# Performance work log

Measured on AMD Instinct MI355X. Metric: run time of the kernel, lower is better.

## Reference

```python
import jax, jax.numpy as jnp
import numpy as np


def setup_inputs() -> dict:
    key = jax.random.key(0)
    k1, k2 = jax.random.split(key)
    embedding = jax.random.normal(k1, (8192, 256), dtype=jnp.float32)
    label = jax.random.randint(k2, (8192,), 0, 1000, dtype=jnp.int64 if jax.config.jax_enable_x64 else jnp.int32)
    return {"embedding": embedding, "label": label}


def reference(embedding, label):
    # embedding: [B, W]; label is unused by the original module's math.
    B, W = embedding.shape
    miu = embedding.mean(axis=0)                      # [W]
    ec = embedding - miu                              # [B, W] centered
    # mean over batch of outer products ec[b] ec[b]^T == (ec^T @ ec) / B
    cov = jnp.einsum('bi,bj->ij', ec, ec) / B         # [W, W]
    diff = cov - jnp.eye(W, dtype=embedding.dtype)
    loss = jnp.sqrt(jnp.sum(diff * diff))             # Frobenius norm
    return loss
```

## Files before the change

### kernel.cpp

```cpp
#include <hip/hip_runtime.h>
#include <math.h>

typedef unsigned int uint32;
typedef unsigned short u16;
typedef __bf16 bf16x8 __attribute__((ext_vector_type(8)));
typedef float f32x16 __attribute__((ext_vector_type(16)));

#define BROWS 8192
#define WDIM 256
#define NT 3
#define CHUNKS 64
#define TILE_ELEMS 16384
#define FIN_BLOCKS 192

#define WS_LOSS 16384
#define WS_DONE 16385
#define WS_PART 16640

__device__ __forceinline__ uint32 pack2bf(float lo, float hi) {
    uint32 a = __float_as_uint(lo), b = __float_as_uint(hi);
    a = (a + 0x7FFFu + ((a >> 16) & 1u)) >> 16;
    b = (b + 0x7FFFu + ((b >> 16) & 1u)) >> 16;
    return (a & 0xFFFFu) | (b << 16);
}
__device__ __forceinline__ u16 f2bf(float x) {
    uint32 a = __float_as_uint(x);
    return (u16)((a + 0x7FFFu + ((a >> 16) & 1u)) >> 16);
}
__device__ __forceinline__ float bflo(uint32 v) { return __uint_as_float(v << 16); }
__device__ __forceinline__ float bfhi(uint32 v) { return __uint_as_float(v & 0xFFFF0000u); }

__device__ __forceinline__ int uswz(int col, int krp) {
    return col * 64 + ((((krp >> 2) ^ (col & 15)) << 2) | (krp & 3));
}

__global__ __launch_bounds__(256)
void gram_fused(const float* __restrict__ E, float* __restrict__ ws) {
    __shared__ uint32 U[WDIM * 64];
    const int t = blockIdx.x, c = blockIdx.y;
    const int tid = threadIdx.x;
    const int ncg = (t == 1) ? 4 : 2;
    const int gcol0 = (t == 2) ? 128 : 0;
    const int row0 = c * 128;
    const int c4 = tid & 15, rp = tid >> 4;

    if (t == 0 && c == 0 && tid < 2) ws[WS_LOSS + tid] = 0.0f;

    for (int cg = 0; cg < ncg; ++cg) {
        const float* Eb = E + (size_t)row0 * WDIM + gcol0 + cg * 64;
        float4 fa[4], fb[4];
        #pragma unroll
        for (int p = 0; p < 4; ++p) {
            const int r0 = 2 * (rp + 16 * p);
            fa[p] = *(const float4*)(Eb + (size_t)r0 * WDIM + c4 * 4);
            fb[p] = *(const float4*)(Eb + (size_t)(r0 + 1) * WDIM + c4 * 4);
        }
        #pragma unroll
        for (int p = 0; p < 4; ++p) {
            const int krp = rp + 16 * p;
            const int colb = cg * 64 + c4 * 4;
            const float av[4] = {fa[p].x, fa[p].y, fa[p].z, fa[p].w};
            const float bv[4] = {fb[p].x, fb[p].y, fb[p].z, fb[p].w};
            #pragma unroll
            for (int i = 0; i < 4; ++i)
                U[uswz(colb + i, krp)] = pack2bf(av[i], bv[i]);
        }
    }
    __syncthreads();

    if (t == 1) {
        const int col = tid;
        float s = 0.f;
        #pragma unroll
        for (int g = 0; g < 16; ++g) {
            const uint4 v = *(const uint4*)&U[col * 64 + ((g ^ (col & 15)) << 2)];
            s += bflo(v.x) + bfhi(v.x) + bflo(v.y) + bfhi(v.y)
               + bflo(v.z) + bfhi(v.z) + bflo(v.w) + bfhi(v.w);
        }
        ws[c * WDIM + col] = s;
    }

    const int w = tid >> 6, l = tid & 63, lm = l & 31;
    const int bBase = (t == 1) ? 128 : 0;
    const int colA = w * 32 + lm;

    f32x16 acc[4];
    #pragma unroll
    for (int n = 0; n < 4; ++n)
        #pragma unroll
        for (int r = 0; r < 16; ++r) acc[n][r] = 0.f;

    #pragma unroll
    for (int s8 = 0; s8 < 8; ++s8) {
        const int grp = 2 * s8 + (l >> 5);
        const bf16x8 a = *(const bf16x8*)&U[colA * 64 + ((grp ^ (colA & 15)) << 2)];
        #pragma unroll
        for (int n = 0; n < 4; ++n) {
            const int colB = bBase + n * 32 + lm;
            const bf16x8 b = *(const bf16x8*)&U[colB * 64 + ((grp ^ (colB & 15)) << 2)];
            acc[n] = __builtin_amdgcn_mfma_f32_32x32x16_bf16(a, b, acc[n], 0, 0, 0);
        }
    }

    u16* part = (u16*)(ws + WS_PART);
    u16* dst = part + ((size_t)c * NT + t) * TILE_ELEMS;
    const int rbase = 32 * w + 4 * (l >> 5);
    #pragma unroll
    for (int n = 0; n < 4; ++n)
        #pragma unroll
        for (int r = 0; r < 16; ++r) {
            const int row = rbase + (r & 3) + 8 * (r >> 2);
            dst[row * 128 + n * 32 + lm] = f2bf(acc[n][r]);
        }
}

__global__ __launch_bounds__(256)
void finalize_kernel(float* __restrict__ ws, float* __restrict__ out) {
    __shared__ float mu[WDIM];
    __shared__ float red[4];
    const u16* part = (const u16*)(ws + WS_PART);
    float* lossacc = ws + WS_LOSS;
    unsigned* done = (unsigned*)(ws + WS_DONE);
    const int tid = threadIdx.x;

    {
        float s = 0.f;
        #pragma unroll 8
        for (int c = 0; c < CHUNKS; ++c) s += ws[c * WDIM + tid];
        mu[tid] = s * (1.0f / (float)BROWS);
    }
    __syncthreads();

    const int e = blockIdx.x * 256 + tid;
    const int t = e >> 14, local = e & 16383;
    const int ti = (t == 2) ? 1 : 0;
    const int tj = (t == 0) ? 0 : 1;
    const int i = ti * 128 + (local >> 7);
    const int j = tj * 128 + (local & 127);

    float g = 0.f;
    #pragma unroll 8
    for (int c = 0; c < CHUNKS; ++c)
        g += bflo((uint32)part[((size_t)c * NT + t) * TILE_ELEMS + local]);

    const float diff = g * (1.0f / (float)BROWS) - mu[i] * mu[j] - ((i == j) ? 1.0f : 0.0f);
    float v = ((t == 1) ? 2.0f : 1.0f) * diff * diff;

    #pragma unroll
    for (int o = 32; o > 0; o >>= 1) v += __shfl_down(v, o, 64);
    if ((tid & 63) == 0) red[tid >> 6] = v;
    __syncthreads();
    if (tid == 0) {
        atomicAdd(lossacc, red[0] + red[1] + red[2] + red[3]);
        __threadfence();
        const unsigned old = atomicAdd(done, 1u);
        if (old == FIN_BLOCKS - 1) {
            __threadfence();
            out[0] = sqrtf(atomicAdd(lossacc, 0.0f));
        }
    }
}

extern "C" void kernel_launch(void* const* d_in, const int* in_sizes, int n_in,
                              void* d_out, int out_size, void* d_ws, size_t ws_size,
                              hipStream_t stream) {
    const float* E = (const float*)d_in[0];
    float* out = (float*)d_out;
    float* ws = (float*)d_ws;

    gram_fused<<<dim3(NT, CHUNKS), 256, 0, stream>>>(E, ws);
    finalize_kernel<<<FIN_BLOCKS, 256, 0, stream>>>(ws, out);
}
```

Baseline: 76.43 us.

## Fuse Gram and finalize kernels with a software grid barrier

Merges the partial-Gram kernel and the finalize kernel into one launch. A global atomic-counter grid barrier separates the two phases, and the mean and loss reduction now run in the same 192 blocks after the barrier. The goal is to remove the second launch and the gap between kernels. In exchange it relies on every block being resident at once, adds spin-wait cost at the barrier, and reuses the shared tile buffer to hold the means.

```diff
diff --git a/kernel.cpp b/kernel.cpp
--- a/kernel.cpp
+++ b/kernel.cpp
@@ -11,11 +11,13 @@
 #define NT 3
 #define CHUNKS 64
 #define TILE_ELEMS 16384
-#define FIN_BLOCKS 192
+#define GRID_BLKS (NT * CHUNKS)
 
 #define WS_LOSS 16384
 #define WS_DONE 16385
 #define WS_PART 16640
+
+__device__ unsigned g_bar1 = 0;
 
 __device__ __forceinline__ uint32 pack2bf(float lo, float hi) {
     uint32 a = __float_as_uint(lo), b = __float_as_uint(hi);
@@ -35,8 +37,10 @@
 }
 
 __global__ __launch_bounds__(256)
-void gram_fused(const float* __restrict__ E, float* __restrict__ ws) {
+void corr_fused(const float* __restrict__ E, float* __restrict__ ws,
+                float* __restrict__ out) {
     __shared__ uint32 U[WDIM * 64];
+    __shared__ float red[4];
     const int t = blockIdx.x, c = blockIdx.y;
     const int tid = threadIdx.x;
     const int ncg = (t == 1) ? 4 : 2;
@@ -112,39 +116,45 @@
             const int row = rbase + (r & 3) + 8 * (r >> 2);
             dst[row * 128 + n * 32 + lm] = f2bf(acc[n][r]);
         }
-}
 
-__global__ __launch_bounds__(256)
-void finalize_kernel(float* __restrict__ ws, float* __restrict__ out) {
-    __shared__ float mu[WDIM];
-    __shared__ float red[4];
-    const u16* part = (const u16*)(ws + WS_PART);
+    __syncthreads();
+    if (tid == 0) {
+        __threadfence();
+        const unsigned old = atomicAdd(&g_bar1, 1u);
+        const unsigned target = old - (old % GRID_BLKS) + GRID_BLKS;
+        while (atomicAdd(&g_bar1, 0u) < target) __builtin_amdgcn_s_sleep(4);
+        __threadfence();
+    }
+    __syncthreads();
+
+    const int b = c * NT + t;
+    float* muS = (float*)U;
+    const u16* partR = (const u16*)(ws + WS_PART);
     float* lossacc = ws + WS_LOSS;
     unsigned* done = (unsigned*)(ws + WS_DONE);
-    const int tid = threadIdx.x;
 
     {
         float s = 0.f;
         #pragma unroll 8
-        for (int c = 0; c < CHUNKS; ++c) s += ws[c * WDIM + tid];
-        mu[tid] = s * (1.0f / (float)BROWS);
+        for (int cc = 0; cc < CHUNKS; ++cc) s += ws[cc * WDIM + tid];
+        muS[tid] = s * (1.0f / (float)BROWS);
     }
     __syncthreads();
 
-    const int e = blockIdx.x * 256 + tid;
-    const int t = e >> 14, local = e & 16383;
-    const int ti = (t == 2) ? 1 : 0;
-    const int tj = (t == 0) ? 0 : 1;
+    const int e = b * 256 + tid;
+    const int tt = e >> 14, local = e & 16383;
+    const int ti = (tt == 2) ? 1 : 0;
+    const int tj = (tt == 0) ? 0 : 1;
     const int i = ti * 128 + (local >> 7);
     const int j = tj * 128 + (local & 127);
 
     float g = 0.f;
     #pragma unroll 8
-    for (int c = 0; c < CHUNKS; ++c)
-        g += bflo((uint32)part[((size_t)c * NT + t) * TILE_ELEMS + local]);
+    for (int cc = 0; cc < CHUNKS; ++cc)
+        g += bflo((uint32)partR[((size_t)cc * NT + tt) * TILE_ELEMS + local]);
 
-    const float diff = g * (1.0f / (float)BROWS) - mu[i] * mu[j] - ((i == j) ? 1.0f : 0.0f);
-    float v = ((t == 1) ? 2.0f : 1.0f) * diff * diff;
+    const float diff = g * (1.0f / (float)BROWS) - muS[i] * muS[j] - ((i == j) ? 1.0f : 0.0f);
+    float v = ((tt == 1) ? 2.0f : 1.0f) * diff * diff;
 
     #pragma unroll
     for (int o = 32; o > 0; o >>= 1) v += __shfl_down(v, o, 64);
@@ -153,8 +163,8 @@
     if (tid == 0) {
         atomicAdd(lossacc, red[0] + red[1] + red[2] + red[3]);
         __threadfence();
-        const unsigned old = atomicAdd(done, 1u);
-        if (old == FIN_BLOCKS - 1) {
+        const unsigned fin = atomicAdd(done, 1u);
+        if (fin == GRID_BLKS - 1) {
             __threadfence();
             out[0] = sqrtf(atomicAdd(lossacc, 0.0f));
         }
@@ -168,6 +178,5 @@
     float* out = (float*)d_out;
     float* ws = (float*)d_ws;
 
-    gram_fused<<<dim3(NT, CHUNKS), 256, 0, stream>>>(E, ws);
-    finalize_kernel<<<FIN_BLOCKS, 256, 0, stream>>>(ws, out);
+    corr_fused<<<dim3(NT, CHUNKS), 256, 0, stream>>>(E, ws, out);
 }
```

Measured after the change: 92.28 us. 1.21x slower.
